# Performance work log

Hardware: AMD Instinct MI355X
Metric: run time of the kernel (lower is better)

The kernel has to match this reference:

```python
import jax, jax.numpy as jnp
import numpy as np
import math

IN_CH = 256
EMBED = 128


def setup_inputs() -> dict:
    key = jax.random.key(0)
    k1, k2, k3, k4, k5 = jax.random.split(key, 5)
    N, C, H, W = 4, IN_CH, 64, 64
    x = jax.random.normal(k1, (N, C, H, W), dtype=jnp.float32)
    # conv1x1 weights stored as [out_ch, in_ch] (kernel is 1x1)
    W_qkv = jax.random.normal(k2, (3 * EMBED, C), dtype=jnp.float32) * (1.0 / math.sqrt(C))
    b_qkv = jax.random.normal(k3, (3 * EMBED,), dtype=jnp.float32) * 0.01
    W_out = jax.random.normal(k4, (C, EMBED), dtype=jnp.float32) * (1.0 / math.sqrt(EMBED))
    b_out = jax.random.normal(k5, (C,), dtype=jnp.float32) * 0.01
    return {"x": x, "W_qkv": W_qkv, "b_qkv": b_qkv, "W_out": W_out, "b_out": b_out}


def reference(x, W_qkv, b_qkv, W_out, b_out):
    N, C, H, W = x.shape
    E = EMBED
    HW = H * W
    # conv1x1 QKV projection: (N, 3E, H, W)
    qkv = jnp.einsum('nchw,oc->nohw', x, W_qkv) + b_qkv[None, :, None, None]
    # faithful RAW C-order reshape (N, 3E, H, W) -> (N, HW, 3E), as in torch .reshape
    qkv = qkv.reshape(N, HW, 3 * E)
    q, k, v = jnp.split(qkv, 3, axis=-1)  # each (N, HW, E)
    # scores scaled by 1/sqrt(H*W), softmax over dim=-2 (columns)
    scores = jnp.einsum('nid,njd->nij', q, k) / math.sqrt(HW)
    soft = jax.nn.softmax(scores, axis=-2)
    out = jnp.einsum('nij,njd->nid', soft, v)  # (N, HW, E)
    # faithful RAW C-order reshape (N, HW, E) -> (N, E, H, W)
    out = out.reshape(N, E, H, W)
    # conv1x1 output projection
    y = jnp.einsum('nehw,ce->nchw', out, W_out) + b_out[None, :, None, None]
    return y
```

## Files before the change

kernel.cpp:

```cpp
#include <hip/hip_runtime.h>
#include <hip/hip_bf16.h>


typedef short bfrag __attribute__((ext_vector_type(8)));
typedef float ffrag __attribute__((ext_vector_type(4)));
typedef unsigned short us4 __attribute__((ext_vector_type(4)));
#define MFMA(a,b,c) __builtin_amdgcn_mfma_f32_16x16x32_bf16((a),(b),(c),0,0,0)

__device__ __forceinline__ unsigned short f2bf(float f){
  union { float f; unsigned u; } v; v.f = f;
  unsigned r = v.u + 0x7fffu + ((v.u >> 16) & 1u);
  return (unsigned short)(r >> 16);
}
__device__ __forceinline__ float bf2f(unsigned short h){
  union { unsigned u; float f; } v; v.u = ((unsigned)h) << 16; return v.f;
}
__device__ __forceinline__ unsigned bfpack(float a, float b){
  return (unsigned)f2bf(a) | ((unsigned)f2bf(b) << 16);
}

__global__ __launch_bounds__(256) void k_wcast(const float* __restrict__ Wq, const float* __restrict__ Wo,
                                               unsigned short* __restrict__ Wqb, unsigned short* __restrict__ Wob){
  int i = blockIdx.x*256 + threadIdx.x;
  if (i < 384*256) Wqb[i] = f2bf(Wq[i]);
  if (i < 256*128) Wob[i] = f2bf(Wo[i]);
}

__global__ __launch_bounds__(256) void k_qkv(const float* __restrict__ x, const unsigned short* __restrict__ Wqb,
                                             const float* __restrict__ bq, unsigned short* __restrict__ qkv){
  constexpr int LD = 136;
  __shared__ __align__(16) unsigned short As[128*LD];
  __shared__ __align__(16) unsigned short Bs[64*LD];
  const int o0 = blockIdx.x*128, h0 = blockIdx.y*64, n = blockIdx.z;
  const int t = threadIdx.x, w = t>>6, lane = t&63, lr = lane&15, q4 = lane>>4;
  ffrag acc[8] = {};
  for (int kh = 0; kh < 2; ++kh) {
    __syncthreads();
    #pragma unroll
    for (int r=0;r<8;++r){
      int pi = t + 256*r; int o = pi>>4, seg = pi&15;
      *(uint4*)&As[o*LD + seg*8] = *(const uint4*)(Wqb + (o0+o)*256 + kh*128 + seg*8);
    }
    #pragma unroll
    for (int r=0;r<8;++r){
      int idx = t + 256*r; int cl = idx>>4, h4 = idx&15;
      float4 v = *(const float4*)(x + (size_t)(n*256 + kh*128 + cl)*4096 + h0 + h4*4);
      Bs[(h4*4+0)*LD + cl] = f2bf(v.x);
      Bs[(h4*4+1)*LD + cl] = f2bf(v.y);
      Bs[(h4*4+2)*LD + cl] = f2bf(v.z);
      Bs[(h4*4+3)*LD + cl] = f2bf(v.w);
    }
    __syncthreads();
    #pragma unroll
    for (int kk=0;kk<4;++kk){
      bfrag a = *(const bfrag*)&Bs[(w*16+lr)*LD + kk*32 + q4*8];
      #pragma unroll
      for (int ot=0;ot<8;++ot){
        bfrag b = *(const bfrag*)&As[(ot*16+lr)*LD + kk*32 + q4*8];
        acc[ot] = MFMA(a,b,acc[ot]);
      }
    }
  }
  size_t base = (size_t)n*384*4096;
  #pragma unroll
  for (int ot=0;ot<8;++ot){
    int o  = o0 + ot*16 + lr;
    float bias = bq[o];
    int hw = h0 + w*16 + q4*4;
    us4 pk;
    pk.x = f2bf(acc[ot][0] + bias); pk.y = f2bf(acc[ot][1] + bias);
    pk.z = f2bf(acc[ot][2] + bias); pk.w = f2bf(acc[ot][3] + bias);
    *(us4*)(qkv + base + (size_t)o*4096 + hw) = pk;
  }
}

__global__ __launch_bounds__(256) void k_stats(const unsigned short* __restrict__ qkv,
                                               float* __restrict__ zp){
  constexpr int LD = 136;
  __shared__ __align__(16) unsigned short Qs[64*LD];
  const int j0 = blockIdx.x*256, ic = blockIdx.y, n = blockIdx.z;
  const int t = threadIdx.x, w = t>>6, lane = t&63, lr = lane&15, q4 = lane>>4;
  size_t base = (size_t)n*384*4096;
  bfrag kf[4][4];
  #pragma unroll
  for (int js=0; js<4; ++js){
    const unsigned short* krow = qkv + base + (size_t)(j0 + w*64 + js*16 + lr)*384 + 128;
    #pragma unroll
    for (int kk=0;kk<4;++kk) kf[js][kk] = *(const bfrag*)(krow + kk*32 + q4*8);
  }
  float Zc[16] = {};
  const float inv64 = 0.015625f;
  for (int rnd=0; rnd<8; ++rnd){
    int i0 = (ic<<9) + rnd*64;
    __syncthreads();
    #pragma unroll
    for (int r=0;r<4;++r){
      int pi = t + 256*r; int il = pi>>4, seg = pi&15;
      *(uint4*)&Qs[il*LD + seg*8] = *(const uint4*)(qkv + base + (size_t)(i0+il)*384 + seg*8);
    }
    __syncthreads();
    #pragma unroll
    for (int it=0; it<4; ++it){
      bfrag qb[4];
      #pragma unroll
      for (int kk=0;kk<4;++kk) qb[kk] = *(const bfrag*)&Qs[(it*16+lr)*LD + kk*32 + q4*8];
      #pragma unroll
      for (int js=0; js<4; ++js){
        ffrag s = {};
        #pragma unroll
        for (int kk=0;kk<4;++kk) s = MFMA(kf[js][kk], qb[kk], s);
        #pragma unroll
        for (int r=0;r<4;++r) Zc[js*4+r] += __expf(s[r]*inv64);
      }
    }
  }
  #pragma unroll
  for (int v=0; v<16; ++v){
    float z = Zc[v];
    z += __shfl_xor(z, 1); z += __shfl_xor(z, 2);
    z += __shfl_xor(z, 4); z += __shfl_xor(z, 8);
    Zc[v] = z;
  }
  if (lr == 0){
    int jb = j0 + w*64;
    float* zrow = zp + (size_t)((n<<3)+ic)*4096;
    #pragma unroll
    for (int js=0; js<4; ++js)
      #pragma unroll
      for (int r=0;r<4;++r)
        zrow[jb + js*16 + q4*4 + r] = Zc[js*4+r];
  }
}

__global__ __launch_bounds__(256) void k_vtrans(const unsigned short* __restrict__ qkv,
                                                const float* __restrict__ zp,
                                                unsigned short* __restrict__ vt){
  constexpr int LD = 136;
  __shared__ __align__(16) unsigned short T[64*LD];
  __shared__ float invZ[64];
  const int p0 = blockIdx.x*64, n = blockIdx.y;
  const int t = threadIdx.x;
  size_t base = (size_t)n*384*4096;
  #pragma unroll
  for (int r=0;r<4;++r){
    int pi = t + 256*r; int pl = pi>>4, seg = pi&15;
    *(uint4*)&T[pl*LD + seg*8] = *(const uint4*)(qkv + base + (size_t)(p0+pl)*384 + 256 + seg*8);
  }
  if (t < 64){
    float Z = 0.f;
    #pragma unroll
    for (int c=0;c<8;++c) Z += zp[(size_t)((n<<3)+c)*4096 + p0 + t];
    invZ[t] = 1.0f / Z;
  }
  __syncthreads();
  unsigned* vt32 = (unsigned*)(vt + (size_t)n*128*4096);
  #pragma unroll
  for (int r=0;r<16;++r){
    int pi = t + 256*r;
    int d = pi>>5, k = pi&31;
    float lo = bf2f(T[(2*k)*LD + d])   * invZ[2*k];
    float hi = bf2f(T[(2*k+1)*LD + d]) * invZ[2*k+1];
    vt32[(size_t)d*2048 + (p0>>1) + k] = bfpack(lo, hi);
  }
}

__global__ __launch_bounds__(256, 2) void k_attn(const unsigned short* __restrict__ qkv,
                                                 const unsigned short* __restrict__ vtg_all,
                                                 unsigned short* __restrict__ part){
  constexpr int LDK = 136, LDV = 72;
  __shared__ __align__(16) unsigned short Ks[2][64*LDK];
  __shared__ __align__(16) unsigned short Vt[2][128*LDV];
  const int i0 = blockIdx.x*128, jh = blockIdx.y, n = blockIdx.z;
  const int t = threadIdx.x, w = t>>6, lane = t&63, lr = lane&15, q4 = lane>>4;
  size_t base = (size_t)n*384*4096;
  const unsigned short* vtg = vtg_all + (size_t)n*128*4096;
  bfrag qf[2][4];
  #pragma unroll
  for (int isub=0;isub<2;++isub){
    const unsigned short* qrow = qkv + base + (size_t)(i0 + w*32 + isub*16 + lr)*384;
    #pragma unroll
    for (int kk=0;kk<4;++kk) qf[isub][kk] = *(const bfrag*)(qrow + kk*32 + q4*8);
  }
  ffrag acc[8][2] = {};
  const float inv64 = 0.015625f;

  const int jl_k = t>>4, seg_k = t&15;
  const int d_v  = t>>3, c_v  = t&7;
  const int sl0 = lr + 16*((2*q4)   & 3);
  const int sl1 = lr + 16*((2*q4+1) & 3);

  {
    const int j0 = jh*1024;
    #pragma unroll
    for (int r=0;r<4;++r)
      *(uint4*)&Ks[0][(jl_k+16*r)*LDK + seg_k*8] =
        *(const uint4*)(qkv + base + (size_t)(j0 + jl_k + 16*r)*384 + 128 + seg_k*8);
    #pragma unroll
    for (int r=0;r<4;++r)
      *(uint4*)&Vt[0][(d_v+32*r)*LDV + c_v*8] =
        *(const uint4*)(vtg + (size_t)(d_v + 32*r)*4096 + j0 + c_v*8);
  }
  __syncthreads();

  for (int it=0; it<16; ++it){
    const int cur = it & 1;
    uint4 kr[4], vr[4];
    if (it < 15){
      const int jn = jh*1024 + (it+1)*64;
      #pragma unroll
      for (int r=0;r<4;++r)
        kr[r] = *(const uint4*)(qkv + base + (size_t)(jn + jl_k + 16*r)*384 + 128 + seg_k*8);
      #pragma unroll
      for (int r=0;r<4;++r)
        vr[r] = *(const uint4*)(vtg + (size_t)(d_v + 32*r)*4096 + jn + c_v*8);
    }
    unsigned pk[4][2][2];
    #pragma unroll
    for (int jt=0;jt<4;++jt){
      bfrag kf[4];
      #pragma unroll
      for (int kk=0;kk<4;++kk) kf[kk] = *(const bfrag*)&Ks[cur][(jt*16+lr)*LDK + kk*32 + q4*8];
      #pragma unroll
      for (int isub=0;isub<2;++isub){
        ffrag s = {};
        #pragma unroll
        for (int kk=0;kk<4;++kk) s = MFMA(kf[kk], qf[isub][kk], s);
        pk[jt][isub][0] = bfpack(__expf(s[0]*inv64), __expf(s[1]*inv64));
        pk[jt][isub][1] = bfpack(__expf(s[2]*inv64), __expf(s[3]*inv64));
      }
    }
    #pragma unroll
    for (int jk=0;jk<2;++jk){
      union { bfrag b; uint4 u; } pf0, pf1;
      unsigned v0[4], v1[4];
      #pragma unroll
      for (int m=0;m<4;++m){
        const int sl = (m<2) ? sl0 : sl1;
        unsigned a0 = __shfl(pk[2*jk  ][0][m&1], sl);
        unsigned b0 = __shfl(pk[2*jk+1][0][m&1], sl);
        v0[m] = (q4 >= 2) ? b0 : a0;
        unsigned a1 = __shfl(pk[2*jk  ][1][m&1], sl);
        unsigned b1 = __shfl(pk[2*jk+1][1][m&1], sl);
        v1[m] = (q4 >= 2) ? b1 : a1;
      }
      pf0.u = make_uint4(v0[0],v0[1],v0[2],v0[3]);
      pf1.u = make_uint4(v1[0],v1[1],v1[2],v1[3]);
      #pragma unroll
      for (int dt=0;dt<8;++dt){
        bfrag af = *(const bfrag*)&Vt[cur][(dt*16+lr)*LDV + jk*32 + q4*8];
        acc[dt][0] = MFMA(af, pf0.b, acc[dt][0]);
        acc[dt][1] = MFMA(af, pf1.b, acc[dt][1]);
      }
    }
    if (it < 15){
      #pragma unroll
      for (int r=0;r<4;++r) *(uint4*)&Ks[cur^1][(jl_k+16*r)*LDK + seg_k*8] = kr[r];
      #pragma unroll
      for (int r=0;r<4;++r) *(uint4*)&Vt[cur^1][(d_v+32*r)*LDV + c_v*8] = vr[r];
      __syncthreads();
    }
  }
  unsigned short* po = part + (size_t)(jh*4+n)*524288;
  #pragma unroll
  for (int isub=0;isub<2;++isub){
    const int i = i0 + w*32 + isub*16 + lr;
    #pragma unroll
    for (int dt=0;dt<8;++dt){
      us4 pko;
      pko.x = f2bf(acc[dt][isub][0]); pko.y = f2bf(acc[dt][isub][1]);
      pko.z = f2bf(acc[dt][isub][2]); pko.w = f2bf(acc[dt][isub][3]);
      *(us4*)(po + (size_t)i*128 + dt*16 + q4*4) = pko;
    }
  }
}

__global__ __launch_bounds__(256) void k_oproj(const unsigned short* __restrict__ part,
                                               const unsigned short* __restrict__ Wob,
                                               const float* __restrict__ bo, float* __restrict__ y){
  constexpr int LD = 136;
  __shared__ __align__(16) unsigned short As[128*LD];
  __shared__ __align__(16) unsigned short Rt[64*LD];
  const int c0 = blockIdx.x*128, h0 = blockIdx.y*64, n = blockIdx.z;
  const int t = threadIdx.x, w = t>>6, lane = t&63, lr = lane&15, q4 = lane>>4;
  #pragma unroll
  for (int r=0;r<8;++r){
    int pi = t + 256*r; int cl = pi>>4, seg = pi&15;
    *(uint4*)&As[cl*LD + seg*8] = *(const uint4*)(Wob + (c0+cl)*128 + seg*8);
  }
  #pragma unroll
  for (int r=0;r<4;++r){
    int pi = t + 256*r; int e = pi>>3, h8 = pi&7;
    size_t f = (size_t)e*4096 + h0 + h8*8;
    float a[8] = {};
    #pragma unroll
    for (int s=0;s<4;++s){
      uint4 u = *(const uint4*)(part + (size_t)(s*4+n)*524288 + f);
      a[0] += bf2f((unsigned short)(u.x & 0xffffu)); a[1] += bf2f((unsigned short)(u.x >> 16));
      a[2] += bf2f((unsigned short)(u.y & 0xffffu)); a[3] += bf2f((unsigned short)(u.y >> 16));
      a[4] += bf2f((unsigned short)(u.z & 0xffffu)); a[5] += bf2f((unsigned short)(u.z >> 16));
      a[6] += bf2f((unsigned short)(u.w & 0xffffu)); a[7] += bf2f((unsigned short)(u.w >> 16));
    }
    #pragma unroll
    for (int k=0;k<8;++k) Rt[(h8*8+k)*LD + e] = f2bf(a[k]);
  }
  __syncthreads();
  ffrag acc[8] = {};
  #pragma unroll
  for (int kk=0;kk<4;++kk){
    bfrag a = *(const bfrag*)&Rt[(w*16+lr)*LD + kk*32 + q4*8];
    #pragma unroll
    for (int cs=0;cs<8;++cs){
      bfrag b = *(const bfrag*)&As[(cs*16+lr)*LD + kk*32 + q4*8];
      acc[cs] = MFMA(a,b,acc[cs]);
    }
  }
  #pragma unroll
  for (int cs=0;cs<8;++cs){
    int c = c0 + cs*16 + lr;
    float bias = bo[c];
    float4 v4 = { acc[cs][0]+bias, acc[cs][1]+bias, acc[cs][2]+bias, acc[cs][3]+bias };
    *(float4*)(y + ((size_t)n*256 + c)*4096 + h0 + w*16 + q4*4) = v4;
  }
}

extern "C" void kernel_launch(void* const* d_in, const int* in_sizes, int n_in,
                              void* d_out, int out_size, void* d_ws, size_t ws_size,
                              hipStream_t stream){
  const float* x  = (const float*)d_in[0];
  const float* Wq = (const float*)d_in[1];
  const float* bq = (const float*)d_in[2];
  const float* Wo = (const float*)d_in[3];
  const float* bo = (const float*)d_in[4];
  float* y = (float*)d_out;
  char* ws = (char*)d_ws;
  unsigned short* qkv  = (unsigned short*)(ws + 0);
  unsigned short* vtg  = (unsigned short*)(ws + 12582912);
  unsigned short* Wqb  = (unsigned short*)(ws + 16777216);
  unsigned short* Wob  = (unsigned short*)(ws + 16973824);
  float* zp   = (float*)(ws + 17039360);
  unsigned short* part = (unsigned short*)(ws + 17629184);

  k_wcast <<<dim3(384),     256, 0, stream>>>(Wq, Wo, Wqb, Wob);
  k_qkv   <<<dim3(3,64,4),  256, 0, stream>>>(x, Wqb, bq, qkv);
  k_stats <<<dim3(16,8,4),  256, 0, stream>>>(qkv, zp);
  k_vtrans<<<dim3(64,4),    256, 0, stream>>>(qkv, zp, vtg);
  k_attn  <<<dim3(32,4,4),  256, 0, stream>>>(qkv, vtg, part);
  k_oproj <<<dim3(2,64,4),  256, 0, stream>>>(part, Wob, bo, y);
}
```

Baseline: 179.9 us.

## Fuse weight casts into GEMMs, swizzle LDS transposes, double-buffer stats Q tiles

Drops the separate weight-cast kernel: k_qkv and k_oproj now read fp32 weights and convert them to bf16 while staging into LDS, removing one launch and a workspace round trip. The transposed LDS stores in k_qkv and k_oproj use an XOR swizzle to reduce bank conflicts on the 2-byte scattered writes. k_stats double-buffers the Q tile, prefetching the next round into registers while computing, so one barrier per round is removed. The cost is redundant weight conversion in every block and extra registers and LDS in k_stats.

```diff
diff --git a/kernel.cpp b/kernel.cpp
--- a/kernel.cpp
+++ b/kernel.cpp
@@ -19,18 +19,12 @@
   return (unsigned)f2bf(a) | ((unsigned)f2bf(b) << 16);
 }
 
-__global__ __launch_bounds__(256) void k_wcast(const float* __restrict__ Wq, const float* __restrict__ Wo,
-                                               unsigned short* __restrict__ Wqb, unsigned short* __restrict__ Wob){
-  int i = blockIdx.x*256 + threadIdx.x;
-  if (i < 384*256) Wqb[i] = f2bf(Wq[i]);
-  if (i < 256*128) Wob[i] = f2bf(Wo[i]);
-}
-
-__global__ __launch_bounds__(256) void k_qkv(const float* __restrict__ x, const unsigned short* __restrict__ Wqb,
+__global__ __launch_bounds__(256) void k_qkv(const float* __restrict__ x, const float* __restrict__ Wq,
                                              const float* __restrict__ bq, unsigned short* __restrict__ qkv){
   constexpr int LD = 136;
   __shared__ __align__(16) unsigned short As[128*LD];
   __shared__ __align__(16) unsigned short Bs[64*LD];
+  char* BsB = (char*)Bs;
   const int o0 = blockIdx.x*128, h0 = blockIdx.y*64, n = blockIdx.z;
   const int t = threadIdx.x, w = t>>6, lane = t&63, lr = lane&15, q4 = lane>>4;
   ffrag acc[8] = {};
@@ -39,21 +33,32 @@
     #pragma unroll
     for (int r=0;r<8;++r){
       int pi = t + 256*r; int o = pi>>4, seg = pi&15;
-      *(uint4*)&As[o*LD + seg*8] = *(const uint4*)(Wqb + (o0+o)*256 + kh*128 + seg*8);
+      const float* wsrc = Wq + (size_t)(o0+o)*256 + kh*128 + seg*8;
+      float4 w0 = *(const float4*)(wsrc);
+      float4 w1 = *(const float4*)(wsrc+4);
+      us4 lo, hv;
+      lo.x=f2bf(w0.x); lo.y=f2bf(w0.y); lo.z=f2bf(w0.z); lo.w=f2bf(w0.w);
+      hv.x=f2bf(w1.x); hv.y=f2bf(w1.y); hv.z=f2bf(w1.z); hv.w=f2bf(w1.w);
+      *(us4*)&As[o*LD + seg*8]     = lo;
+      *(us4*)&As[o*LD + seg*8 + 4] = hv;
     }
     #pragma unroll
     for (int r=0;r<8;++r){
       int idx = t + 256*r; int cl = idx>>4, h4 = idx&15;
       float4 v = *(const float4*)(x + (size_t)(n*256 + kh*128 + cl)*4096 + h0 + h4*4);
-      Bs[(h4*4+0)*LD + cl] = f2bf(v.x);
-      Bs[(h4*4+1)*LD + cl] = f2bf(v.y);
-      Bs[(h4*4+2)*LD + cl] = f2bf(v.z);
-      Bs[(h4*4+3)*LD + cl] = f2bf(v.w);
+      float vv[4] = {v.x, v.y, v.z, v.w};
+      #pragma unroll
+      for (int u=0;u<4;++u){
+        int row = h4*4+u;
+        *(unsigned short*)(BsB + row*272 + ((2*cl) ^ (((row>>3)&7)<<4))) = f2bf(vv[u]);
+      }
     }
     __syncthreads();
+    const int arow = w*16+lr;
+    const int akey = ((arow>>3)&7)<<4;
     #pragma unroll
     for (int kk=0;kk<4;++kk){
-      bfrag a = *(const bfrag*)&Bs[(w*16+lr)*LD + kk*32 + q4*8];
+      bfrag a = *(const bfrag*)(BsB + arow*272 + ((kk*64 + q4*16) ^ akey));
       #pragma unroll
       for (int ot=0;ot<8;++ot){
         bfrag b = *(const bfrag*)&As[(ot*16+lr)*LD + kk*32 + q4*8];
@@ -74,10 +79,10 @@
   }
 }
 
-__global__ __launch_bounds__(256) void k_stats(const unsigned short* __restrict__ qkv,
-                                               float* __restrict__ zp){
+__global__ __launch_bounds__(256, 2) void k_stats(const unsigned short* __restrict__ qkv,
+                                                  float* __restrict__ zp){
   constexpr int LD = 136;
-  __shared__ __align__(16) unsigned short Qs[64*LD];
+  __shared__ __align__(16) unsigned short Qs[2][64*LD];
   const int j0 = blockIdx.x*256, ic = blockIdx.y, n = blockIdx.z;
   const int t = threadIdx.x, w = t>>6, lane = t&63, lr = lane&15, q4 = lane>>4;
   size_t base = (size_t)n*384*4096;
@@ -88,22 +93,32 @@
     #pragma unroll
     for (int kk=0;kk<4;++kk) kf[js][kk] = *(const bfrag*)(krow + kk*32 + q4*8);
   }
+  const int il = t>>4, seg = t&15;
+  {
+    const int i0 = (ic<<9);
+    #pragma unroll
+    for (int r=0;r<4;++r)
+      *(uint4*)&Qs[0][(il+16*r)*LD + seg*8] =
+        *(const uint4*)(qkv + base + (size_t)(i0+il+16*r)*384 + seg*8);
+  }
+  __syncthreads();
   float Zc[16] = {};
   const float inv64 = 0.015625f;
   for (int rnd=0; rnd<8; ++rnd){
-    int i0 = (ic<<9) + rnd*64;
-    __syncthreads();
-    #pragma unroll
-    for (int r=0;r<4;++r){
-      int pi = t + 256*r; int il = pi>>4, seg = pi&15;
-      *(uint4*)&Qs[il*LD + seg*8] = *(const uint4*)(qkv + base + (size_t)(i0+il)*384 + seg*8);
-    }
-    __syncthreads();
+    const int cur = rnd&1;
+    uint4 qr[4];
+    if (rnd<7){
+      const int i1 = (ic<<9) + (rnd+1)*64;
+      #pragma unroll
+      for (int r=0;r<4;++r)
+        qr[r] = *(const uint4*)(qkv + base + (size_t)(i1+il+16*r)*384 + seg*8);
+    }
+    const unsigned short* qs = Qs[cur];
     #pragma unroll
     for (int it=0; it<4; ++it){
       bfrag qb[4];
       #pragma unroll
-      for (int kk=0;kk<4;++kk) qb[kk] = *(const bfrag*)&Qs[(it*16+lr)*LD + kk*32 + q4*8];
+      for (int kk=0;kk<4;++kk) qb[kk] = *(const bfrag*)&qs[(it*16+lr)*LD + kk*32 + q4*8];
       #pragma unroll
       for (int js=0; js<4; ++js){
         ffrag s = {};
@@ -112,6 +127,11 @@
         #pragma unroll
         for (int r=0;r<4;++r) Zc[js*4+r] += __expf(s[r]*inv64);
       }
+    }
+    if (rnd<7){
+      #pragma unroll
+      for (int r=0;r<4;++r) *(uint4*)&Qs[cur^1][(il+16*r)*LD + seg*8] = qr[r];
+      __syncthreads();
     }
   }
   #pragma unroll
@@ -275,17 +295,25 @@
 }
 
 __global__ __launch_bounds__(256) void k_oproj(const unsigned short* __restrict__ part,
-                                               const unsigned short* __restrict__ Wob,
+                                               const float* __restrict__ Wo,
                                                const float* __restrict__ bo, float* __restrict__ y){
   constexpr int LD = 136;
   __shared__ __align__(16) unsigned short As[128*LD];
   __shared__ __align__(16) unsigned short Rt[64*LD];
+  char* RtB = (char*)Rt;
   const int c0 = blockIdx.x*128, h0 = blockIdx.y*64, n = blockIdx.z;
   const int t = threadIdx.x, w = t>>6, lane = t&63, lr = lane&15, q4 = lane>>4;
   #pragma unroll
   for (int r=0;r<8;++r){
     int pi = t + 256*r; int cl = pi>>4, seg = pi&15;
-    *(uint4*)&As[cl*LD + seg*8] = *(const uint4*)(Wob + (c0+cl)*128 + seg*8);
+    const float* wsrc = Wo + (size_t)(c0+cl)*128 + seg*8;
+    float4 w0 = *(const float4*)(wsrc);
+    float4 w1 = *(const float4*)(wsrc+4);
+    us4 lo, hv;
+    lo.x=f2bf(w0.x); lo.y=f2bf(w0.y); lo.z=f2bf(w0.z); lo.w=f2bf(w0.w);
+    hv.x=f2bf(w1.x); hv.y=f2bf(w1.y); hv.z=f2bf(w1.z); hv.w=f2bf(w1.w);
+    *(us4*)&As[cl*LD + seg*8]     = lo;
+    *(us4*)&As[cl*LD + seg*8 + 4] = hv;
   }
   #pragma unroll
   for (int r=0;r<4;++r){
@@ -301,13 +329,18 @@
       a[6] += bf2f((unsigned short)(u.w & 0xffffu)); a[7] += bf2f((unsigned short)(u.w >> 16));
     }
     #pragma unroll
-    for (int k=0;k<8;++k) Rt[(h8*8+k)*LD + e] = f2bf(a[k]);
+    for (int u2=0;u2<8;++u2){
+      int row = h8*8+u2;
+      *(unsigned short*)(RtB + row*272 + ((2*e) ^ (((row>>3)&7)<<4))) = f2bf(a[u2]);
+    }
   }
   __syncthreads();
   ffrag acc[8] = {};
+  const int arow = w*16+lr;
+  const int akey = ((arow>>3)&7)<<4;
   #pragma unroll
   for (int kk=0;kk<4;++kk){
-    bfrag a = *(const bfrag*)&Rt[(w*16+lr)*LD + kk*32 + q4*8];
+    bfrag a = *(const bfrag*)(RtB + arow*272 + ((kk*64 + q4*16) ^ akey));
     #pragma unroll
     for (int cs=0;cs<8;++cs){
       bfrag b = *(const bfrag*)&As[(cs*16+lr)*LD + kk*32 + q4*8];
@@ -335,15 +368,12 @@
   char* ws = (char*)d_ws;
   unsigned short* qkv  = (unsigned short*)(ws + 0);
   unsigned short* vtg  = (unsigned short*)(ws + 12582912);
-  unsigned short* Wqb  = (unsigned short*)(ws + 16777216);
-  unsigned short* Wob  = (unsigned short*)(ws + 16973824);
   float* zp   = (float*)(ws + 17039360);
   unsigned short* part = (unsigned short*)(ws + 17629184);
 
-  k_wcast <<<dim3(384),     256, 0, stream>>>(Wq, Wo, Wqb, Wob);
-  k_qkv   <<<dim3(3,64,4),  256, 0, stream>>>(x, Wqb, bq, qkv);
+  k_qkv   <<<dim3(3,64,4),  256, 0, stream>>>(x, Wq, bq, qkv);
   k_stats <<<dim3(16,8,4),  256, 0, stream>>>(qkv, zp);
   k_vtrans<<<dim3(64,4),    256, 0, stream>>>(qkv, zp, vtg);
   k_attn  <<<dim3(32,4,4),  256, 0, stream>>>(qkv, vtg, part);
-  k_oproj <<<dim3(2,64,4),  256, 0, stream>>>(part, Wob, bo, y);
-}
+  k_oproj <<<dim3(2,64,4),  256, 0, stream>>>(part, Wo, bo, y);
+}
```

Result: no change. 182.2 us (+1.3%).
